# Kernel optimization log

Measured on AMD Instinct MI355X. Metric: run time of the kernel, lower is better.

The kernel has to match this reference:

```python
import jax, jax.numpy as jnp
import numpy as np
import math

D_MODEL = 1024
NUM_HEADS = 16
D_K = 64
B, T = 2, 2048


def setup_inputs() -> dict:
    key = jax.random.key(0)
    ks = jax.random.split(key, 12)
    s = 0.02
    return {
        "Q": jax.random.normal(ks[0], (B, T, D_MODEL), jnp.float32),
        "K": jax.random.normal(ks[1], (B, T, D_MODEL), jnp.float32),
        "V": jax.random.normal(ks[2], (B, T, D_MODEL), jnp.float32),
        # stacked per-head projection weights: [H, d_model, d_k]
        "Wq": jax.random.normal(ks[3], (NUM_HEADS, D_MODEL, D_K), jnp.float32) * s,
        "bq": jax.random.normal(ks[4], (NUM_HEADS, D_K), jnp.float32) * s,
        "Wk": jax.random.normal(ks[5], (NUM_HEADS, D_MODEL, D_K), jnp.float32) * s,
        "bk": jax.random.normal(ks[6], (NUM_HEADS, D_K), jnp.float32) * s,
        "Wv": jax.random.normal(ks[7], (NUM_HEADS, D_MODEL, D_K), jnp.float32) * s,
        "bv": jax.random.normal(ks[8], (NUM_HEADS, D_K), jnp.float32) * s,
        "Wo": jax.random.normal(ks[9], (D_MODEL, D_MODEL), jnp.float32) * s,
        "bo": jax.random.normal(ks[10], (D_MODEL,), jnp.float32) * s,
    }


def reference(Q, K, V, Wq, bq, Wk, bk, Wv, bv, Wo, bo):
    scale = 1.0 / math.sqrt(D_K)
    # fused batched per-head projections (replaces the Python per-head loop)
    Qh = jnp.einsum("btd,hdk->bhtk", Q, Wq) + bq[None, :, None, :]
    Kh = jnp.einsum("btd,hdk->bhtk", K, Wk) + bk[None, :, None, :]
    Vh = jnp.einsum("btd,hdk->bhtk", V, Wv) + bv[None, :, None, :]
    scores = jnp.einsum("bhtk,bhsk->bhts", Qh, Kh) * scale  # [B,H,T,T]
    attn = jax.nn.softmax(scores, axis=-1)
    ctx = jnp.einsum("bhts,bhsk->bhtk", attn, Vh)  # [B,H,T,d_k]
    # Faithful to the original: plain view of contiguous [B,H,T,d] into
    # [B,T,H*d] WITHOUT transposing head/time (matches torch .view semantics).
    bsz, nt = Q.shape[0], Q.shape[1]
    x = ctx.reshape(bsz, nt, NUM_HEADS * D_K)
    out = x @ Wo.T + bo
    # dropout with p=0.0 is identity; omitted for determinism
    return out
```

## Files before the change

kernel.cpp:

```cpp
#include <hip/hip_runtime.h>
#include <stdint.h>

typedef __attribute__((ext_vector_type(8))) short short8;
typedef __attribute__((ext_vector_type(4))) short short4v;
typedef __attribute__((ext_vector_type(4))) float float4v;

#define MFMA16(a, b, c) __builtin_amdgcn_mfma_f32_16x16x32_bf16((a), (b), (c), 0, 0, 0)

__device__ __forceinline__ ushort f2bf_rne(float f) {
  union { float f; unsigned u; } x; x.f = f;
  unsigned r = x.u + 0x7FFFu + ((x.u >> 16) & 1u);
  return (ushort)(r >> 16);
}
__device__ __forceinline__ ushort f2bf_trunc(float f) {
  union { float f; unsigned u; } x; x.f = f;
  return (ushort)(x.u >> 16);
}
__device__ __forceinline__ void gload16(const ushort* g, ushort* lds) {
  __builtin_amdgcn_global_load_lds(
      (__attribute__((address_space(1))) unsigned int*)g,
      (__attribute__((address_space(3))) unsigned int*)lds, 16, 0, 0);
}

#define CEXP 0.1803368801111204f

__device__ __forceinline__ void transpose64f(const float* __restrict__ in, int is,
                                             ushort* __restrict__ out, int os,
                                             ushort* lds ) {
  const int t = threadIdx.x;
#pragma unroll
  for (int it = 0; it < 2; ++it) {
    int e = it * 2048 + t * 8;
    int r = e >> 6, c = e & 63;
    const float* p = in + (size_t)r * is + c;
    float4 x0 = *(const float4*)p;
    float4 x1 = *(const float4*)(p + 4);
    ushort tv[8] __attribute__((aligned(16))) = {
        f2bf_rne(x0.x), f2bf_rne(x0.y), f2bf_rne(x0.z), f2bf_rne(x0.w),
        f2bf_rne(x1.x), f2bf_rne(x1.y), f2bf_rne(x1.z), f2bf_rne(x1.w)};
    *(uint4*)&lds[r * 72 + c] = *(const uint4*)tv;
  }
  __syncthreads();
  const int cc = t >> 2;
  const int rg = (t & 3) * 16;
  ushort tmp[16] __attribute__((aligned(16)));
#pragma unroll
  for (int i = 0; i < 16; ++i) tmp[i] = lds[(rg + i) * 72 + cc];
  *(uint4*)&out[(size_t)cc * os + rg] = *(const uint4*)&tmp[0];
  *(uint4*)&out[(size_t)cc * os + rg + 8] = *(const uint4*)&tmp[8];
}

__global__ __launch_bounds__(256) void prep_kernel(
    const float* __restrict__ Q, const float* __restrict__ K,
    const float* __restrict__ V, const float* __restrict__ Wo,
    const float* __restrict__ Wq, const float* __restrict__ Wk,
    const float* __restrict__ Wv, ushort* __restrict__ Qb, ushort* __restrict__ Kb,
    ushort* __restrict__ Vb, ushort* __restrict__ WoB, ushort* __restrict__ BtQ,
    ushort* __restrict__ BtK, ushort* __restrict__ BtV) {
  __shared__ ushort lds[64 * 72];
  const int bx = blockIdx.x;
  if (bx < 6656) {
    const float* s;
    ushort* d;
    int i;
    if (bx < 6144) {
      const int plane = bx >> 11;
      s = plane == 0 ? Q : (plane == 1 ? K : V);
      d = plane == 0 ? Qb : (plane == 1 ? Kb : Vb);
      i = ((bx & 2047) * 256 + threadIdx.x) * 8;
    } else {
      s = Wo;
      d = WoB;
      i = ((bx - 6144) * 256 + threadIdx.x) * 8;
    }
    float4 a = *(const float4*)(s + i);
    float4 b = *(const float4*)(s + i + 4);
    ushort t[8] __attribute__((aligned(16))) = {
        f2bf_rne(a.x), f2bf_rne(a.y), f2bf_rne(a.z), f2bf_rne(a.w),
        f2bf_rne(b.x), f2bf_rne(b.y), f2bf_rne(b.z), f2bf_rne(b.w)};
    *(uint4*)(d + i) = *(const uint4*)t;
  } else {
    const int rb = bx - 6656;
    const int dt = rb & 15, h = (rb >> 4) & 15, z = rb >> 8;
    const float* W = z == 0 ? Wq : (z == 1 ? Wk : Wv);
    ushort* Bt = z == 0 ? BtQ : (z == 1 ? BtK : BtV);
    transpose64f(W + h * 65536 + dt * 4096, 64, Bt + h * 65536 + dt * 64, 1024, lds);
  }
}

__global__ __launch_bounds__(256, 2) void repack_w_kernel(
    const float* __restrict__ Wq, const float* __restrict__ Wk,
    const float* __restrict__ Wv, ushort* __restrict__ BtQ, ushort* __restrict__ BtK,
    ushort* __restrict__ BtV) {
  __shared__ ushort lds[64 * 72];
  const float* W = blockIdx.z == 0 ? Wq : (blockIdx.z == 1 ? Wk : Wv);
  ushort* Bt = blockIdx.z == 0 ? BtQ : (blockIdx.z == 1 ? BtK : BtV);
  const int h = blockIdx.y, dt = blockIdx.x;
  transpose64f(W + h * 65536 + dt * 4096, 64, Bt + h * 65536 + dt * 64, 1024, lds);
}

template <int F32>
__device__ __forceinline__ void stage16(const void* G, size_t eoff, ushort* ldst) {
  if (F32) {
    const float* p = (const float*)G + eoff;
    float4 x0 = *(const float4*)p;
    float4 x1 = *(const float4*)(p + 4);
    ushort t[8] __attribute__((aligned(16))) = {
        f2bf_rne(x0.x), f2bf_rne(x0.y), f2bf_rne(x0.z), f2bf_rne(x0.w),
        f2bf_rne(x1.x), f2bf_rne(x1.y), f2bf_rne(x1.z), f2bf_rne(x1.w)};
    *(uint4*)ldst = *(const uint4*)t;
  } else {
    gload16((const ushort*)G + eoff, ldst);
  }
}

template <int AF32, int BF32>
__device__ __forceinline__ void gemm_body_basic(const void* __restrict__ A,
                                                const void* __restrict__ Bt,
                                                const float* __restrict__ bias,
                                                void* __restrict__ C, int cmode,
                                                float ascale, int N, int K, ushort* lA,
                                                ushort* lB) {
  const int tid = threadIdx.x;
  const int l = tid & 63, lane15 = l & 15, quad = l >> 4;
  const int mbase = blockIdx.y * 128, nbase = blockIdx.x * 128;
  const int w = tid >> 6;
  const int wrow = (w >> 1) * 64, wcol = (w & 1) * 64;
  const int e0 = tid * 8;
  const int e1 = 2048 + tid * 8;
  const int r0 = e0 >> 5, c0 = e0 & 31;
  const int r1 = e1 >> 5, c1 = e1 & 31;

  float4v acc[4][4];
#pragma unroll
  for (int i = 0; i < 4; ++i)
#pragma unroll
    for (int j = 0; j < 4; ++j) acc[i][j] = (float4v){0.f, 0.f, 0.f, 0.f};

  for (int kb = 0; kb < K; kb += 32) {
    __syncthreads();
    stage16<AF32>(A, (size_t)(mbase + r0) * K + c0 + kb, &lA[e0]);
    stage16<AF32>(A, (size_t)(mbase + r1) * K + c1 + kb, &lA[e1]);
    stage16<BF32>(Bt, (size_t)(nbase + r0) * K + c0 + kb, &lB[e0]);
    stage16<BF32>(Bt, (size_t)(nbase + r1) * K + c1 + kb, &lB[e1]);
    asm volatile("s_waitcnt vmcnt(0)" ::: "memory");
    __syncthreads();
    short8 a[4], b[4];
#pragma unroll
    for (int i = 0; i < 4; ++i) {
      a[i] = *(const short8*)&lA[(wrow + i * 16 + lane15) * 32 + quad * 8];
      b[i] = *(const short8*)&lB[(wcol + i * 16 + lane15) * 32 + quad * 8];
    }
#pragma unroll
    for (int i = 0; i < 4; ++i)
#pragma unroll
      for (int j = 0; j < 4; ++j) acc[i][j] = MFMA16(a[i], b[j], acc[i][j]);
  }

  if (cmode == 3) {
    __syncthreads();
    uint* sp = (uint*)lA + w * 576;
    const int bb = mbase >> 11;
    const int tb = (mbase & 2047) + wrow;
#pragma unroll
    for (int j = 0; j < 4; ++j) {
      {
        const int n = nbase + wcol + j * 16 + lane15;
        const float bvs = bias[n];
#pragma unroll
        for (int i = 0; i < 4; ++i)
#pragma unroll
          for (int rp = 0; rp < 2; ++rp) {
            const uint lo = f2bf_rne((acc[i][j][2 * rp] + bvs) * ascale);
            const uint hi = f2bf_rne((acc[i][j][2 * rp + 1] + bvs) * ascale);
            sp[36 * lane15 + i * 8 + quad * 2 + rp] = lo | (hi << 16);
          }
      }
#pragma unroll
      for (int t = 0; t < 2; ++t) {
        const int row = t * 8 + (l >> 3);
        const int c = l & 7;
        uint4 d = *(const uint4*)(sp + 36 * row + 4 * c);
        const int ng = nbase + wcol + j * 16 + row;
        ushort* dst = (ushort*)C + ((size_t)(bb * 1024 + ng)) * 2048 + tb + c * 8;
        *(uint4*)dst = d;
      }
    }
    return;
  }

#pragma unroll
  for (int j = 0; j < 4; ++j) {
    const int n = nbase + wcol + j * 16 + lane15;
    const float bvs = bias[n];
#pragma unroll
    for (int i = 0; i < 4; ++i) {
      const int m0 = mbase + wrow + i * 16 + quad * 4;
#pragma unroll
      for (int r = 0; r < 4; ++r) {
        const float val = (acc[i][j][r] + bvs) * ascale;
        if (cmode == 1) {
          const int m = m0 + r;
          const int bb = m >> 11, t = m & 2047;
          ((ushort*)C)[((size_t)(bb * 1024 + n)) * 2048 + t] = f2bf_rne(val);
        } else if (cmode == 2) {
          ((float*)C)[(size_t)(m0 + r) * N + n] = val;
        } else {
          ((ushort*)C)[(size_t)(m0 + r) * N + n] = f2bf_rne(val);
        }
      }
    }
  }
}

__global__ __launch_bounds__(256, 2) void proj3_kernel(
    const ushort* __restrict__ Qb, const ushort* __restrict__ Kb,
    const ushort* __restrict__ Vb, const ushort* __restrict__ BtQ,
    const ushort* __restrict__ BtK, const ushort* __restrict__ BtV,
    const float* __restrict__ bq, const float* __restrict__ bk,
    const float* __restrict__ bv, ushort* __restrict__ Qh, ushort* __restrict__ Kh,
    ushort* __restrict__ Vt) {
  __shared__ ushort lA[5120], lB[4096];
  if (blockIdx.z == 0)
    gemm_body_basic<0, 0>(Qb, BtQ, bq, Qh, 0, CEXP, 1024, 1024, lA, lB);
  else if (blockIdx.z == 1)
    gemm_body_basic<0, 0>(Kb, BtK, bk, Kh, 0, 1.0f, 1024, 1024, lA, lB);
  else
    gemm_body_basic<0, 0>(Vb, BtV, bv, Vt, 3, 1.0f, 1024, 1024, lA, lB);
}

__global__ __launch_bounds__(256, 2) void gemm_out_kernel(
    const ushort* __restrict__ X, const ushort* __restrict__ WoB,
    const float* __restrict__ bo, float* __restrict__ out) {
  __shared__ ushort lA[4096], lB[2048];
  const int tid = threadIdx.x;
  const int l = tid & 63, lane15 = l & 15, quad = l >> 4;
  const int mbase = blockIdx.y * 128, nbase = blockIdx.x * 64;
  const int wv = tid >> 6;
  const int wrow = wv * 32;
  const int e0 = tid * 8;
  const int e1 = 2048 + tid * 8;
  const int r0 = e0 >> 5, c0 = e0 & 31;
  const int r1 = e1 >> 5, c1 = e1 & 31;
  const ushort* Ag0 = X + (size_t)(mbase + r0) * 1024 + c0;
  const ushort* Ag1 = X + (size_t)(mbase + r1) * 1024 + c1;
  const ushort* Bg0 = WoB + (size_t)(nbase + r0) * 1024 + c0;

  float4v acc[2][4];
#pragma unroll
  for (int i = 0; i < 2; ++i)
#pragma unroll
    for (int j = 0; j < 4; ++j) acc[i][j] = (float4v){0.f, 0.f, 0.f, 0.f};

  for (int kb = 0; kb < 1024; kb += 32) {
    __syncthreads();
    gload16(Ag0 + kb, &lA[e0]);
    gload16(Ag1 + kb, &lA[e1]);
    gload16(Bg0 + kb, &lB[e0]);
    asm volatile("s_waitcnt vmcnt(0)" ::: "memory");
    __syncthreads();
    short8 a[2], b[4];
#pragma unroll
    for (int i = 0; i < 2; ++i)
      a[i] = *(const short8*)&lA[(wrow + i * 16 + lane15) * 32 + quad * 8];
#pragma unroll
    for (int j = 0; j < 4; ++j)
      b[j] = *(const short8*)&lB[(j * 16 + lane15) * 32 + quad * 8];
#pragma unroll
    for (int i = 0; i < 2; ++i)
#pragma unroll
      for (int j = 0; j < 4; ++j) acc[i][j] = MFMA16(a[i], b[j], acc[i][j]);
  }

#pragma unroll
  for (int j = 0; j < 4; ++j) {
    const int n = nbase + j * 16 + lane15;
    const float bvs = bo[n];
#pragma unroll
    for (int i = 0; i < 2; ++i) {
      const int m0 = mbase + wrow + i * 16 + quad * 4;
#pragma unroll
      for (int r = 0; r < 4; ++r) out[(size_t)(m0 + r) * 1024 + n] = acc[i][j][r] + bvs;
    }
  }
}

__global__ __launch_bounds__(256, 2) void proj3f_kernel(
    const float* __restrict__ Q, const float* __restrict__ Kin,
    const float* __restrict__ V, const ushort* __restrict__ BtQ,
    const ushort* __restrict__ BtK, const ushort* __restrict__ BtV,
    const float* __restrict__ bq, const float* __restrict__ bk,
    const float* __restrict__ bv, ushort* __restrict__ Qh, ushort* __restrict__ Kh,
    ushort* __restrict__ Vt) {
  __shared__ ushort lA[5120], lB[4096];
  if (blockIdx.z == 0)
    gemm_body_basic<1, 0>(Q, BtQ, bq, Qh, 0, CEXP, 1024, 1024, lA, lB);
  else if (blockIdx.z == 1)
    gemm_body_basic<1, 0>(Kin, BtK, bk, Kh, 0, 1.0f, 1024, 1024, lA, lB);
  else
    gemm_body_basic<1, 0>(V, BtV, bv, Vt, 3, 1.0f, 1024, 1024, lA, lB);
}

__global__ __launch_bounds__(256, 2) void gemm_btf_kernel(
    const ushort* __restrict__ X, const float* __restrict__ Wo,
    const float* __restrict__ bo, float* __restrict__ out) {
  __shared__ ushort lA[5120], lB[4096];
  gemm_body_basic<0, 1>(X, Wo, bo, out, 2, 1.0f, 1024, 1024, lA, lB);
}

__global__ __launch_bounds__(512, 4) void attn_kernel(const ushort* __restrict__ Qh,
                                                      const ushort* __restrict__ Kh,
                                                      const ushort* __restrict__ Vt,
                                                      ushort* __restrict__ ctxout) {
  __shared__ ushort lK[2][64 * 64];
  __shared__ ushort lV[2][64 * 64];
  const int tid = threadIdx.x, l = tid & 63, wv = tid >> 6;
  const int lane15 = l & 15, quad = l >> 4;
  const int bh = blockIdx.x, b = bh >> 4, h = bh & 15;
  const int q0 = blockIdx.y * 128 + wv * 16;

  const int sr = tid >> 3;
  const int scb = (tid & 7) ^ (sr & 7);
  const ushort* Kp = Kh + (size_t)(b * 2048) * 1024 + h * 64;
  const ushort* Vp = Vt + (size_t)(bh * 64) * 2048;
  const ushort* Kg = Kp + (size_t)sr * 1024 + scb * 8;
  const ushort* Vg = Vp + (size_t)sr * 2048 + scb * 8;

  const ushort* qrow = Qh + (size_t)(b * 2048 + q0 + lane15) * 1024 + h * 64;
  const short8 qa0 = *(const short8*)&qrow[quad * 8];
  const short8 qa1 = *(const short8*)&qrow[32 + quad * 8];

  const int xm = lane15 & 7;
  const int fr0 = lane15 * 64 + ((quad ^ xm) * 8);
  const int fr1 = lane15 * 64 + (((quad + 4) ^ xm) * 8);

  const short8 ones = {0x3F80, 0x3F80, 0x3F80, 0x3F80, 0x3F80, 0x3F80, 0x3F80, 0x3F80};

  float4v o[4];
  float4v lf = (float4v){0.f, 0.f, 0.f, 0.f};
#pragma unroll
  for (int i = 0; i < 4; ++i) o[i] = (float4v){0.f, 0.f, 0.f, 0.f};

  gload16(Kg, &lK[0][tid * 8]);
  gload16(Vg, &lV[0][tid * 8]);
  asm volatile("s_waitcnt vmcnt(0)" ::: "memory");
  __syncthreads();

  int cur = 0;
  for (int s0 = 0; s0 < 2048; s0 += 64) {
    if (s0 + 64 < 2048) {
      gload16(Kg + (size_t)(s0 + 64) * 1024, &lK[cur ^ 1][tid * 8]);
      gload16(Vg + (s0 + 64), &lV[cur ^ 1][tid * 8]);
    }
    const ushort* Kl = &lK[cur][0];
    const ushort* Vl = &lV[cur][0];

    float4v sb[4];
    __builtin_amdgcn_s_setprio(1);
#pragma unroll
    for (int i = 0; i < 4; ++i) {
      short8 k0 = *(const short8*)&Kl[i * 1024 + fr0];
      short8 k1 = *(const short8*)&Kl[i * 1024 + fr1];
      float4v c = (float4v){0.f, 0.f, 0.f, 0.f};
      c = MFMA16(k0, qa0, c);
      c = MFMA16(k1, qa1, c);
      sb[i] = c;
    }
    __builtin_amdgcn_s_setprio(0);

    uint wpk[4][2];
#pragma unroll
    for (int i = 0; i < 4; ++i) {
      const float e0 = __builtin_amdgcn_exp2f(sb[i][0]);
      const float e1 = __builtin_amdgcn_exp2f(sb[i][1]);
      const float e2 = __builtin_amdgcn_exp2f(sb[i][2]);
      const float e3 = __builtin_amdgcn_exp2f(sb[i][3]);
      asm("v_cvt_pk_bf16_f32 %0, %1, %2" : "=v"(wpk[i][0]) : "v"(e0), "v"(e1));
      asm("v_cvt_pk_bf16_f32 %0, %1, %2" : "=v"(wpk[i][1]) : "v"(e2), "v"(e3));
    }

    union PK { uint w[4]; short8 v; };
    PK u0, u1;
    {
      uint a0 = wpk[0][0], b0 = wpk[1][0];
      asm("v_permlane32_swap_b32 %0, %1" : "+v"(a0), "+v"(b0));
      asm("v_permlane16_swap_b32 %0, %1" : "+v"(a0), "+v"(b0));
      uint a1 = wpk[0][1], b1 = wpk[1][1];
      asm("v_permlane32_swap_b32 %0, %1" : "+v"(a1), "+v"(b1));
      asm("v_permlane16_swap_b32 %0, %1" : "+v"(a1), "+v"(b1));
      u0.w[0] = a0; u0.w[1] = a1; u0.w[2] = b0; u0.w[3] = b1;
      uint a2 = wpk[2][0], b2 = wpk[3][0];
      asm("v_permlane32_swap_b32 %0, %1" : "+v"(a2), "+v"(b2));
      asm("v_permlane16_swap_b32 %0, %1" : "+v"(a2), "+v"(b2));
      uint a3 = wpk[2][1], b3 = wpk[3][1];
      asm("v_permlane32_swap_b32 %0, %1" : "+v"(a3), "+v"(b3));
      asm("v_permlane16_swap_b32 %0, %1" : "+v"(a3), "+v"(b3));
      u1.w[0] = a2; u1.w[1] = a3; u1.w[2] = b2; u1.w[3] = b3;
    }
    const short8 pa0 = u0.v;
    const short8 pa1 = u1.v;

    __builtin_amdgcn_s_setprio(1);
    lf = MFMA16(pa0, ones, lf);
    lf = MFMA16(pa1, ones, lf);
#pragma unroll
    for (int nf = 0; nf < 4; ++nf) {
      short8 v0 = *(const short8*)&Vl[nf * 1024 + fr0];
      short8 v1 = *(const short8*)&Vl[nf * 1024 + fr1];
      o[nf] = MFMA16(pa0, v0, o[nf]);
      o[nf] = MFMA16(pa1, v1, o[nf]);
    }
    __builtin_amdgcn_s_setprio(0);

    asm volatile("s_waitcnt vmcnt(0)" ::: "memory");
    __syncthreads();
    cur ^= 1;
  }

  float inv[4];
#pragma unroll
  for (int r = 0; r < 4; ++r) inv[r] = (lf[r] > 0.f) ? 1.0f / lf[r] : 0.0f;
  ushort* crow = ctxout + ((size_t)bh * 2048 + q0) * 64;
#pragma unroll
  for (int nf = 0; nf < 4; ++nf)
#pragma unroll
    for (int r = 0; r < 4; ++r)
      crow[(size_t)(quad * 4 + r) * 64 + nf * 16 + lane15] = f2bf_rne(o[nf][r] * inv[r]);
}

extern "C" void kernel_launch(void* const* d_in, const int* in_sizes, int n_in,
                              void* d_out, int out_size, void* d_ws, size_t ws_size,
                              hipStream_t stream) {
  const float* Q = (const float*)d_in[0];
  const float* K = (const float*)d_in[1];
  const float* V = (const float*)d_in[2];
  const float* Wq = (const float*)d_in[3];
  const float* bq = (const float*)d_in[4];
  const float* Wk = (const float*)d_in[5];
  const float* bk = (const float*)d_in[6];
  const float* Wv = (const float*)d_in[7];
  const float* bv = (const float*)d_in[8];
  const float* Wo = (const float*)d_in[9];
  const float* bo = (const float*)d_in[10];
  float* out = (float*)d_out;
  ushort* ws = (ushort*)d_ws;

  if (ws_size >= (58ull << 20)) {
    ushort* Qh = ws;
    ushort* Kh = Qh + (4 << 20);
    ushort* Vt = Kh + (4 << 20);
    ushort* BtQ = Vt + (4 << 20);
    ushort* BtK = BtQ + (1 << 20);
    ushort* BtV = BtK + (1 << 20);
    ushort* X = BtQ;
    ushort* WoB = ws + (16ull << 20);
    ushort* Qb = WoB + (1 << 20);
    ushort* Kb = Qb + (4 << 20);
    ushort* Vb = Kb + (4 << 20);

    prep_kernel<<<dim3(7424), 256, 0, stream>>>(Q, K, V, Wo, Wq, Wk, Wv, Qb, Kb, Vb,
                                                WoB, BtQ, BtK, BtV);
    proj3_kernel<<<dim3(8, 32, 3), 256, 0, stream>>>(Qb, Kb, Vb, BtQ, BtK, BtV, bq, bk,
                                                     bv, Qh, Kh, Vt);
    attn_kernel<<<dim3(32, 16), 512, 0, stream>>>(Qh, Kh, Vt, X);
    gemm_out_kernel<<<dim3(16, 32), 256, 0, stream>>>(X, WoB, bo, out);
  } else {
    ushort* Qh = ws;
    ushort* Kh = Qh + (4 << 20);
    ushort* Vt = Kh + (4 << 20);
    ushort* R = Vt + (4 << 20);
    ushort* BtQ = R;
    ushort* BtK = R + (1 << 20);
    ushort* BtV = R + (2 << 20);
    ushort* X = R;

    repack_w_kernel<<<dim3(16, 16, 3), 256, 0, stream>>>(Wq, Wk, Wv, BtQ, BtK, BtV);
    proj3f_kernel<<<dim3(8, 32, 3), 256, 0, stream>>>(Q, K, V, BtQ, BtK, BtV, bq, bk, bv,
                                                      Qh, Kh, Vt);
    attn_kernel<<<dim3(32, 16), 512, 0, stream>>>(Qh, Kh, Vt, X);
    gemm_btf_kernel<<<dim3(8, 32), 256, 0, stream>>>(X, Wo, bo, out);
  }
}
```

Measured before the change: 219.2 us.

## Double-buffer LDS tiles in projection and output GEMM k-loops

New measurement: 220.9 us. Within noise of the previous version (+0.8%).

```diff
diff --git a/kernel.cpp b/kernel.cpp
--- a/kernel.cpp
+++ b/kernel.cpp
@@ -137,24 +137,37 @@
 #pragma unroll
     for (int j = 0; j < 4; ++j) acc[i][j] = (float4v){0.f, 0.f, 0.f, 0.f};
 
+  stage16<AF32>(A, (size_t)(mbase + r0) * K + c0, &lA[e0]);
+  stage16<AF32>(A, (size_t)(mbase + r1) * K + c1, &lA[e1]);
+  stage16<BF32>(Bt, (size_t)(nbase + r0) * K + c0, &lB[e0]);
+  stage16<BF32>(Bt, (size_t)(nbase + r1) * K + c1, &lB[e1]);
+  asm volatile("s_waitcnt vmcnt(0)" ::: "memory");
+  __syncthreads();
+
+  int cur = 0;
   for (int kb = 0; kb < K; kb += 32) {
-    __syncthreads();
-    stage16<AF32>(A, (size_t)(mbase + r0) * K + c0 + kb, &lA[e0]);
-    stage16<AF32>(A, (size_t)(mbase + r1) * K + c1 + kb, &lA[e1]);
-    stage16<BF32>(Bt, (size_t)(nbase + r0) * K + c0 + kb, &lB[e0]);
-    stage16<BF32>(Bt, (size_t)(nbase + r1) * K + c1 + kb, &lB[e1]);
+    const int nxt = cur ^ 1;
+    if (kb + 32 < K) {
+      stage16<AF32>(A, (size_t)(mbase + r0) * K + c0 + kb + 32, &lA[nxt * 4096 + e0]);
+      stage16<AF32>(A, (size_t)(mbase + r1) * K + c1 + kb + 32, &lA[nxt * 4096 + e1]);
+      stage16<BF32>(Bt, (size_t)(nbase + r0) * K + c0 + kb + 32, &lB[nxt * 4096 + e0]);
+      stage16<BF32>(Bt, (size_t)(nbase + r1) * K + c1 + kb + 32, &lB[nxt * 4096 + e1]);
+    }
+    const ushort* cA = &lA[cur * 4096];
+    const ushort* cB = &lB[cur * 4096];
+    short8 a[4], b[4];
+#pragma unroll
+    for (int i = 0; i < 4; ++i) {
+      a[i] = *(const short8*)&cA[(wrow + i * 16 + lane15) * 32 + quad * 8];
+      b[i] = *(const short8*)&cB[(wcol + i * 16 + lane15) * 32 + quad * 8];
+    }
+#pragma unroll
+    for (int i = 0; i < 4; ++i)
+#pragma unroll
+      for (int j = 0; j < 4; ++j) acc[i][j] = MFMA16(a[i], b[j], acc[i][j]);
     asm volatile("s_waitcnt vmcnt(0)" ::: "memory");
     __syncthreads();
-    short8 a[4], b[4];
-#pragma unroll
-    for (int i = 0; i < 4; ++i) {
-      a[i] = *(const short8*)&lA[(wrow + i * 16 + lane15) * 32 + quad * 8];
-      b[i] = *(const short8*)&lB[(wcol + i * 16 + lane15) * 32 + quad * 8];
-    }
-#pragma unroll
-    for (int i = 0; i < 4; ++i)
-#pragma unroll
-      for (int j = 0; j < 4; ++j) acc[i][j] = MFMA16(a[i], b[j], acc[i][j]);
+    cur = nxt;
   }
 
   if (cmode == 3) {
@@ -220,7 +233,7 @@
     const float* __restrict__ bq, const float* __restrict__ bk,
     const float* __restrict__ bv, ushort* __restrict__ Qh, ushort* __restrict__ Kh,
     ushort* __restrict__ Vt) {
-  __shared__ ushort lA[5120], lB[4096];
+  __shared__ ushort lA[8192], lB[8192];
   if (blockIdx.z == 0)
     gemm_body_basic<0, 0>(Qb, BtQ, bq, Qh, 0, CEXP, 1024, 1024, lA, lB);
   else if (blockIdx.z == 1)
@@ -232,7 +245,7 @@
 __global__ __launch_bounds__(256, 2) void gemm_out_kernel(
     const ushort* __restrict__ X, const ushort* __restrict__ WoB,
     const float* __restrict__ bo, float* __restrict__ out) {
-  __shared__ ushort lA[4096], lB[2048];
+  __shared__ ushort lA[8192], lB[4096];
   const int tid = threadIdx.x;
   const int l = tid & 63, lane15 = l & 15, quad = l >> 4;
   const int mbase = blockIdx.y * 128, nbase = blockIdx.x * 64;
@@ -252,24 +265,36 @@
 #pragma unroll
     for (int j = 0; j < 4; ++j) acc[i][j] = (float4v){0.f, 0.f, 0.f, 0.f};
 
+  gload16(Ag0, &lA[e0]);
+  gload16(Ag1, &lA[e1]);
+  gload16(Bg0, &lB[e0]);
+  asm volatile("s_waitcnt vmcnt(0)" ::: "memory");
+  __syncthreads();
+
+  int cur = 0;
   for (int kb = 0; kb < 1024; kb += 32) {
-    __syncthreads();
-    gload16(Ag0 + kb, &lA[e0]);
-    gload16(Ag1 + kb, &lA[e1]);
-    gload16(Bg0 + kb, &lB[e0]);
+    const int nxt = cur ^ 1;
+    if (kb + 32 < 1024) {
+      gload16(Ag0 + kb + 32, &lA[nxt * 4096 + e0]);
+      gload16(Ag1 + kb + 32, &lA[nxt * 4096 + e1]);
+      gload16(Bg0 + kb + 32, &lB[nxt * 2048 + e0]);
+    }
+    const ushort* cA = &lA[cur * 4096];
+    const ushort* cB = &lB[cur * 2048];
+    short8 a[2], b[4];
+#pragma unroll
+    for (int i = 0; i < 2; ++i)
+      a[i] = *(const short8*)&cA[(wrow + i * 16 + lane15) * 32 + quad * 8];
+#pragma unroll
+    for (int j = 0; j < 4; ++j)
+      b[j] = *(const short8*)&cB[(j * 16 + lane15) * 32 + quad * 8];
+#pragma unroll
+    for (int i = 0; i < 2; ++i)
+#pragma unroll
+      for (int j = 0; j < 4; ++j) acc[i][j] = MFMA16(a[i], b[j], acc[i][j]);
     asm volatile("s_waitcnt vmcnt(0)" ::: "memory");
     __syncthreads();
-    short8 a[2], b[4];
-#pragma unroll
-    for (int i = 0; i < 2; ++i)
-      a[i] = *(const short8*)&lA[(wrow + i * 16 + lane15) * 32 + quad * 8];
-#pragma unroll
-    for (int j = 0; j < 4; ++j)
-      b[j] = *(const short8*)&lB[(j * 16 + lane15) * 32 + quad * 8];
-#pragma unroll
-    for (int i = 0; i < 2; ++i)
-#pragma unroll
-      for (int j = 0; j < 4; ++j) acc[i][j] = MFMA16(a[i], b[j], acc[i][j]);
+    cur = nxt;
   }
 
 #pragma unroll
@@ -292,7 +317,7 @@
     const float* __restrict__ bq, const float* __restrict__ bk,
     const float* __restrict__ bv, ushort* __restrict__ Qh, ushort* __restrict__ Kh,
     ushort* __restrict__ Vt) {
-  __shared__ ushort lA[5120], lB[4096];
+  __shared__ ushort lA[8192], lB[8192];
   if (blockIdx.z == 0)
     gemm_body_basic<1, 0>(Q, BtQ, bq, Qh, 0, CEXP, 1024, 1024, lA, lB);
   else if (blockIdx.z == 1)
@@ -304,7 +329,7 @@
 __global__ __launch_bounds__(256, 2) void gemm_btf_kernel(
     const ushort* __restrict__ X, const float* __restrict__ Wo,
     const float* __restrict__ bo, float* __restrict__ out) {
-  __shared__ ushort lA[5120], lB[4096];
+  __shared__ ushort lA[8192], lB[8192];
   gemm_body_basic<0, 1>(X, Wo, bo, out, 2, 1.0f, 1024, 1024, lA, lB);
 }
 
```
